# Performance work log

Hardware: AMD Instinct MI355X
Metric: run time of the kernel (lower is better)

## Reference

```python
import jax, jax.numpy as jnp
import numpy as np

N_NODES = 100000    # nodes in river network
N_PATHS = 1000000   # number of (src, dst) routing paths
MAX_DELAY = 16
DT = 1.0
CASCADE = 1.0
T = int(MAX_DELAY / DT)        # expanded time window (assert in original)
E = 8000000                    # total flattened path-node entries


def setup_inputs() -> dict:
    key = jax.random.key(0)
    k1, k2, k3 = jax.random.split(key, 3)
    params = jax.random.uniform(k1, (N_NODES,), dtype=jnp.float32)
    path_idxs = jnp.sort(jax.random.randint(k2, (E,), 0, N_PATHS, dtype=jnp.int32))
    path_nodes = jax.random.randint(k3, (E,), 0, N_NODES, dtype=jnp.int32)
    return {"params": params, "path_idxs": path_idxs, "path_nodes": path_nodes}


def reference(params, path_idxs, path_nodes):
    # irf_fn 'linear_storage': per-node linear-reservoir impulse response h(t)=exp(-t/k)/k
    k = params + 0.5                                  # storage const in [0.5, 1.5)
    t = jnp.arange(T, dtype=params.dtype) * DT        # [T]
    irfs = jnp.exp(-t[None, :] / k[:, None]) / k[:, None]   # [N, T]
    # frequency domain
    irfs_freq = jnp.fft.rfft(irfs, n=T, axis=-1)      # [N, F] complex
    # irf_agg 'log_triton': cascade-combine IRFs along each path = product of
    # transfer functions, done in log domain: gather logs, segment-sum per path.
    log_freq = jnp.log(irfs_freq)                     # [N, F] complex log
    gathered = log_freq[path_nodes]                   # [E, F] irregular gather
    agg_re = jax.ops.segment_sum(gathered.real, path_idxs, num_segments=N_PATHS)
    agg_im = jax.ops.segment_sum(gathered.imag, path_idxs, num_segments=N_PATHS)
    agg_log = (agg_re + 1j * agg_im) * CASCADE        # [P, F]
    irfs_freq_agg = jnp.exp(agg_log)
    # back to time domain
    irfs_agg = jnp.fft.irfft(irfs_freq_agg, n=T, axis=-1)   # [P, T]
    irfs_agg = jax.nn.relu(irfs_agg)
    irfs_agg = jnp.flip(irfs_agg, -1)                 # sampler.phi_k is identity for dt=1
    irfs_agg = irfs_agg / jnp.sum(irfs_agg, -1, keepdims=True)
    return irfs_agg                                   # COO values; coords scatter is a storage step
```

## Files before the change

kernel.cpp:

```cpp
#include <hip/hip_runtime.h>
#include <math.h>

#define N_NODES  100000
#define N_PATHS  1000000
#define E_TOT    8000000
#define NF       9
#define TAB_U32  25000
#define PN_CHUNK 10240
#define BLK      1024

#define RMIN 0.135330f
#define RMAX 0.513420f
#define QSCALE (255.0f / (RMAX - RMIN))
#define DEQ    ((RMAX - RMIN) / 255.0f)

__device__ __constant__ float COS16[16] = {
  1.0f,  0.92387953f,  0.70710678f,  0.38268343f,  0.0f, -0.38268343f, -0.70710678f, -0.92387953f,
 -1.0f, -0.92387953f, -0.70710678f, -0.38268343f,  0.0f,  0.38268343f,  0.70710678f,  0.92387953f };
__device__ __constant__ float SIN16[16] = {
  0.0f,  0.38268343f,  0.70710678f,  0.92387953f,  1.0f,  0.92387953f,  0.70710678f,  0.38268343f,
  0.0f, -0.38268343f, -0.70710678f, -0.92387953f, -1.0f, -0.92387953f, -0.70710678f, -0.38268343f };

__global__ void node_rq_kernel(const float* __restrict__ params,
                               unsigned char* __restrict__ rtab_q) {
    int n = blockIdx.x * blockDim.x + threadIdx.x;
    if (n >= N_NODES) return;
    float k = params[n] + 0.5f;
    float r = expf(-1.0f / k);
    float q = (r - RMIN) * QSCALE;
    q = fminf(fmaxf(q + 0.5f, 0.0f), 255.0f);
    rtab_q[n] = (unsigned char)q;
}

__device__ __forceinline__ void put_bounds(int a, int b, int e, int* __restrict__ start) {
    for (int p = a + 1; p <= b; ++p) start[p] = e;
}
__global__ void seg_starts_kernel(const int* __restrict__ pidx,
                                  int* __restrict__ start) {
    int q = blockIdx.x * blockDim.x + threadIdx.x;
    if (q >= E_TOT / 4) return;
    int e = q * 4;
    int4 v = ((const int4*)pidx)[q];
    int prev = (e == 0) ? -1 : pidx[e - 1];
    put_bounds(prev, v.x, e,     start);
    put_bounds(v.x,  v.y, e + 1, start);
    put_bounds(v.y,  v.z, e + 2, start);
    put_bounds(v.z,  v.w, e + 3, start);
    if (e + 4 == E_TOT) {
        for (int p = v.w + 1; p <= N_PATHS; ++p) start[p] = E_TOT;
    }
}

__global__ __launch_bounds__(BLK) void path_kernel(const int* __restrict__ start,
                                                   const int* __restrict__ pnode,
                                                   const unsigned int* __restrict__ rtab_q,
                                                   float* __restrict__ out) {
    __shared__ unsigned int tab[TAB_U32];
    __shared__ int pn[PN_CHUNK];
    const unsigned char* tabb = (const unsigned char*)tab;

    int tid = threadIdx.x;
    for (int i = tid; i < TAB_U32; i += BLK) tab[i] = rtab_q[i];

    int p0 = blockIdx.x * BLK;
    int p  = p0 + tid;
    int pend = (p0 + BLK < N_PATHS) ? p0 + BLK : N_PATHS;

    int blk_s = start[p0];
    int blk_e = start[pend];
    int s0 = 0, s1 = 0;
    if (p < N_PATHS) { s0 = start[p]; s1 = start[p + 1]; }

    float d0 = 1.0f, d8 = 1.0f;
    float dr[7], di[7];
#pragma unroll
    for (int f = 0; f < 7; f++) { dr[f] = 1.0f; di[f] = 0.0f; }

    for (int base = blk_s; base < blk_e; base += PN_CHUNK) {
        int len = (blk_e - base < PN_CHUNK) ? (blk_e - base) : PN_CHUNK;
        __syncthreads();
        for (int i = tid; i < len; i += BLK) pn[i] = pnode[base + i];
        __syncthreads();

        int lo = (s0 > base) ? s0 : base;
        int hi = (s1 < base + len) ? s1 : base + len;
        int e = lo;
        for (; e + 1 < hi; e += 2) {
            int na = pn[e - base];
            int nb = pn[e + 1 - base];
            float ra = fmaf((float)tabb[na], DEQ, RMIN);
            float rb = fmaf((float)tabb[nb], DEQ, RMIN);
#pragma unroll
            for (int f = 1; f <= 7; f++) {
                float cf = COS16[f], sf = SIN16[f];
                float t1r = fmaf(-ra, cf, 1.0f), t1i = ra * sf;
                float t2r = fmaf(-rb, cf, 1.0f), t2i = rb * sf;
                float tr = fmaf(t1r, t2r, -t1i * t2i);
                float ti = fmaf(t1r, t2i,  t1i * t2r);
                float a = dr[f - 1], b = di[f - 1];
                dr[f - 1] = fmaf(a, tr, -b * ti);
                di[f - 1] = fmaf(a, ti,  b * tr);
            }
            d0 *= (1.0f - ra) * (1.0f - rb);
            d8 *= (1.0f + ra) * (1.0f + rb);
        }
        if (e < hi) {
            int nn = pn[e - base];
            float r = fmaf((float)tabb[nn], DEQ, RMIN);
#pragma unroll
            for (int f = 1; f <= 7; f++) {
                float cf = COS16[f], sf = SIN16[f];
                float tr = fmaf(-r, cf, 1.0f), ti = r * sf;
                float a = dr[f - 1], b = di[f - 1];
                dr[f - 1] = fmaf(a, tr, -b * ti);
                di[f - 1] = fmaf(a, ti,  b * tr);
            }
            d0 = fmaf(-d0, r, d0);
            d8 = fmaf( d8, r, d8);
        }
    }

    if (p >= N_PATHS) return;

    float Xr[NF], Xi[NF];
    Xr[0] = 1.0f; Xi[0] = 0.0f;
#pragma unroll
    for (int f = 1; f < 8; f++) {
        float a = dr[f - 1], b = di[f - 1];
        float m = fmaf(a, a, b * b);
        float inv = d0 * __builtin_amdgcn_rcpf(m);
        Xr[f] =  a * inv;
        Xi[f] = -b * inv;
    }
    Xr[8] = d0 * __builtin_amdgcn_rcpf(d8); Xi[8] = 0.0f;

    float xt[16];
    float ssum = 0.0f;
#pragma unroll
    for (int t = 0; t < 16; t++) {
        float acc = Xr[0] + ((t & 1) ? -Xr[8] : Xr[8]);
#pragma unroll
        for (int f = 1; f < 8; f++) {
            int kk = (f * t) & 15;
            acc = fmaf(2.0f * Xr[f], COS16[kk], acc);
            acc = fmaf(-2.0f * Xi[f], SIN16[kk], acc);
        }
        acc *= (1.0f / 16.0f);
        acc = fmaxf(acc, 0.0f);
        xt[t] = acc;
        ssum += acc;
    }

    float invs = __builtin_amdgcn_rcpf(ssum);
    float4* op4 = (float4*)(out + (size_t)p * 16);
    op4[0] = make_float4(xt[15] * invs, xt[14] * invs, xt[13] * invs, xt[12] * invs);
    op4[1] = make_float4(xt[11] * invs, xt[10] * invs, xt[9]  * invs, xt[8]  * invs);
    op4[2] = make_float4(xt[7]  * invs, xt[6]  * invs, xt[5]  * invs, xt[4]  * invs);
    op4[3] = make_float4(xt[3]  * invs, xt[2]  * invs, xt[1]  * invs, xt[0]  * invs);
}

extern "C" void kernel_launch(void* const* d_in, const int* in_sizes, int n_in,
                              void* d_out, int out_size, void* d_ws, size_t ws_size,
                              hipStream_t stream) {
    const float* params = (const float*)d_in[0];
    const int* path_idxs = (const int*)d_in[1];
    const int* path_nodes = (const int*)d_in[2];
    float* out = (float*)d_out;

    size_t off_rq    = 0;
    size_t off_start = (off_rq + (size_t)N_NODES + 1023) & ~(size_t)1023;

    unsigned char* rtab_q = (unsigned char*)d_ws + off_rq;
    int* start = (int*)((char*)d_ws + off_start);

    {
        int threads = 256;
        int blocks = (N_NODES + threads - 1) / threads;
        node_rq_kernel<<<blocks, threads, 0, stream>>>(params, rtab_q);
    }
    {
        int threads = 256;
        int blocks = (E_TOT / 4 + threads - 1) / threads;
        seg_starts_kernel<<<blocks, threads, 0, stream>>>(path_idxs, start);
    }
    {
        int blocks = (N_PATHS + BLK - 1) / BLK;
        path_kernel<<<blocks, BLK, 0, stream>>>(start, path_nodes,
                                                (const unsigned int*)rtab_q, out);
    }
}
```

Baseline: 161.6 us.

## Pre-gather quantized node values per entry and batch four factors per step

The segment-start pass now also gathers each entry's quantized reservoir value into a byte array, so the path kernel streams 1 byte per entry instead of 4-byte node ids plus an LDS table lookup. The path kernel shrinks to 256-thread blocks without the 100KB table in shared memory, which allows more blocks per CU. It also multiplies four (1 - r z^-1) factors at once through their elementary symmetric polynomials instead of pairwise products, cutting per-entry FLOPs. The cost is an extra 8MB written and read back, plus a 100KB LDS table load in each block of the first pass.

```diff
diff --git a/kernel.cpp b/kernel.cpp
--- a/kernel.cpp
+++ b/kernel.cpp
@@ -6,8 +6,10 @@
 #define E_TOT    8000000
 #define NF       9
 #define TAB_U32  25000
-#define PN_CHUNK 10240
-#define BLK      1024
+#define EB       1024
+#define EPT      2
+#define PB       256
+#define RCH      4096
 
 #define RMIN 0.135330f
 #define RMAX 0.513420f
@@ -35,36 +37,51 @@
 __device__ __forceinline__ void put_bounds(int a, int b, int e, int* __restrict__ start) {
     for (int p = a + 1; p <= b; ++p) start[p] = e;
 }
-__global__ void seg_starts_kernel(const int* __restrict__ pidx,
-                                  int* __restrict__ start) {
-    int q = blockIdx.x * blockDim.x + threadIdx.x;
-    if (q >= E_TOT / 4) return;
-    int e = q * 4;
-    int4 v = ((const int4*)pidx)[q];
-    int prev = (e == 0) ? -1 : pidx[e - 1];
-    put_bounds(prev, v.x, e,     start);
-    put_bounds(v.x,  v.y, e + 1, start);
-    put_bounds(v.y,  v.z, e + 2, start);
-    put_bounds(v.z,  v.w, e + 3, start);
-    if (e + 4 == E_TOT) {
-        for (int p = v.w + 1; p <= N_PATHS; ++p) start[p] = E_TOT;
-    }
-}
-
-__global__ __launch_bounds__(BLK) void path_kernel(const int* __restrict__ start,
+
+__global__ __launch_bounds__(EB) void epass_kernel(const int* __restrict__ pidx,
                                                    const int* __restrict__ pnode,
                                                    const unsigned int* __restrict__ rtab_q,
-                                                   float* __restrict__ out) {
+                                                   int* __restrict__ start,
+                                                   unsigned char* __restrict__ r8_all) {
     __shared__ unsigned int tab[TAB_U32];
-    __shared__ int pn[PN_CHUNK];
     const unsigned char* tabb = (const unsigned char*)tab;
-
     int tid = threadIdx.x;
-    for (int i = tid; i < TAB_U32; i += BLK) tab[i] = rtab_q[i];
-
-    int p0 = blockIdx.x * BLK;
+    for (int i = tid; i < TAB_U32; i += EB) tab[i] = rtab_q[i];
+    __syncthreads();
+
+    int base_q = blockIdx.x * EB * EPT;
+#pragma unroll
+    for (int g = 0; g < EPT; g++) {
+        int q = base_q + g * EB + tid;
+        if (q >= E_TOT / 4) break;
+        int e = q * 4;
+        int4 v = ((const int4*)pidx)[q];
+        int4 w = ((const int4*)pnode)[q];
+        uchar4 r;
+        r.x = tabb[w.x];
+        r.y = tabb[w.y];
+        r.z = tabb[w.z];
+        r.w = tabb[w.w];
+        ((uchar4*)r8_all)[q] = r;
+        int prev = (e == 0) ? -1 : pidx[e - 1];
+        put_bounds(prev, v.x, e,     start);
+        put_bounds(v.x,  v.y, e + 1, start);
+        put_bounds(v.y,  v.z, e + 2, start);
+        put_bounds(v.z,  v.w, e + 3, start);
+        if (e + 4 == E_TOT) {
+            for (int p = v.w + 1; p <= N_PATHS; ++p) start[p] = E_TOT;
+        }
+    }
+}
+
+__global__ __launch_bounds__(PB) void path_kernel(const int* __restrict__ start,
+                                                  const unsigned char* __restrict__ r8_all,
+                                                  float* __restrict__ out) {
+    __shared__ unsigned char rch[RCH + 4];
+    int tid = threadIdx.x;
+    int p0 = blockIdx.x * PB;
     int p  = p0 + tid;
-    int pend = (p0 + BLK < N_PATHS) ? p0 + BLK : N_PATHS;
+    int pend = (p0 + PB < N_PATHS) ? p0 + PB : N_PATHS;
 
     int blk_s = start[p0];
     int blk_e = start[pend];
@@ -76,47 +93,46 @@
 #pragma unroll
     for (int f = 0; f < 7; f++) { dr[f] = 1.0f; di[f] = 0.0f; }
 
-    for (int base = blk_s; base < blk_e; base += PN_CHUNK) {
-        int len = (blk_e - base < PN_CHUNK) ? (blk_e - base) : PN_CHUNK;
+    const unsigned int* r8w = (const unsigned int*)r8_all;
+    for (int ab = blk_s & ~3; ab < blk_e; ab += RCH) {
+        int wlen = (blk_e - ab < RCH) ? (blk_e - ab) : RCH;
+        int nw = (wlen + 3) >> 2;
         __syncthreads();
-        for (int i = tid; i < len; i += BLK) pn[i] = pnode[base + i];
+        for (int j = tid; j < nw; j += PB)
+            ((unsigned int*)rch)[j] = r8w[(ab >> 2) + j];
         __syncthreads();
 
-        int lo = (s0 > base) ? s0 : base;
-        int hi = (s1 < base + len) ? s1 : base + len;
-        int e = lo;
-        for (; e + 1 < hi; e += 2) {
-            int na = pn[e - base];
-            int nb = pn[e + 1 - base];
-            float ra = fmaf((float)tabb[na], DEQ, RMIN);
-            float rb = fmaf((float)tabb[nb], DEQ, RMIN);
+        int lo = (s0 > ab) ? s0 : ab;
+        int hi = (s1 < ab + wlen) ? s1 : ab + wlen;
+        int n = hi - lo;
+        int bi = lo - ab;
+        for (int j = 0; j < n; j += 4) {
+            float ra = fmaf((float)rch[bi + j], DEQ, RMIN);
+            float rb = (j + 1 < n) ? fmaf((float)rch[bi + j + 1], DEQ, RMIN) : 0.0f;
+            float rc = (j + 2 < n) ? fmaf((float)rch[bi + j + 2], DEQ, RMIN) : 0.0f;
+            float rd = (j + 3 < n) ? fmaf((float)rch[bi + j + 3], DEQ, RMIN) : 0.0f;
+            float sab = ra + rb, qab = ra * rb;
+            float scd = rc + rd, qcd = rc * rd;
+            float e1 = sab + scd;
+            float e2 = fmaf(sab, scd, qab + qcd);
+            float e3 = fmaf(qab, scd, qcd * sab);
+            float e4 = qab * qcd;
 #pragma unroll
             for (int f = 1; f <= 7; f++) {
-                float cf = COS16[f], sf = SIN16[f];
-                float t1r = fmaf(-ra, cf, 1.0f), t1i = ra * sf;
-                float t2r = fmaf(-rb, cf, 1.0f), t2i = rb * sf;
-                float tr = fmaf(t1r, t2r, -t1i * t2i);
-                float ti = fmaf(t1r, t2i,  t1i * t2r);
+                float tr = fmaf(-e1, COS16[f], 1.0f);
+                tr = fmaf( e2, COS16[(2 * f) & 15], tr);
+                tr = fmaf(-e3, COS16[(3 * f) & 15], tr);
+                tr = fmaf( e4, COS16[(4 * f) & 15], tr);
+                float ti = e1 * SIN16[f];
+                ti = fmaf(-e2, SIN16[(2 * f) & 15], ti);
+                ti = fmaf( e3, SIN16[(3 * f) & 15], ti);
+                ti = fmaf(-e4, SIN16[(4 * f) & 15], ti);
                 float a = dr[f - 1], b = di[f - 1];
                 dr[f - 1] = fmaf(a, tr, -b * ti);
                 di[f - 1] = fmaf(a, ti,  b * tr);
             }
-            d0 *= (1.0f - ra) * (1.0f - rb);
-            d8 *= (1.0f + ra) * (1.0f + rb);
-        }
-        if (e < hi) {
-            int nn = pn[e - base];
-            float r = fmaf((float)tabb[nn], DEQ, RMIN);
-#pragma unroll
-            for (int f = 1; f <= 7; f++) {
-                float cf = COS16[f], sf = SIN16[f];
-                float tr = fmaf(-r, cf, 1.0f), ti = r * sf;
-                float a = dr[f - 1], b = di[f - 1];
-                dr[f - 1] = fmaf(a, tr, -b * ti);
-                di[f - 1] = fmaf(a, ti,  b * tr);
-            }
-            d0 = fmaf(-d0, r, d0);
-            d8 = fmaf( d8, r, d8);
+            d0 *= ((1.0f - e1) + (e2 - e3)) + e4;
+            d8 *= ((1.0f + e1) + (e2 + e3)) + e4;
         }
     }
 
@@ -169,9 +185,11 @@
 
     size_t off_rq    = 0;
     size_t off_start = (off_rq + (size_t)N_NODES + 1023) & ~(size_t)1023;
+    size_t off_r8    = (off_start + (size_t)(N_PATHS + 1) * 4 + 1023) & ~(size_t)1023;
 
     unsigned char* rtab_q = (unsigned char*)d_ws + off_rq;
     int* start = (int*)((char*)d_ws + off_start);
+    unsigned char* r8_all = (unsigned char*)d_ws + off_r8;
 
     {
         int threads = 256;
@@ -179,13 +197,14 @@
         node_rq_kernel<<<blocks, threads, 0, stream>>>(params, rtab_q);
     }
     {
-        int threads = 256;
-        int blocks = (E_TOT / 4 + threads - 1) / threads;
-        seg_starts_kernel<<<blocks, threads, 0, stream>>>(path_idxs, start);
+        int per_block = EB * EPT;
+        int blocks = (E_TOT / 4 + per_block - 1) / per_block;
+        epass_kernel<<<blocks, EB, 0, stream>>>(path_idxs, path_nodes,
+                                                (const unsigned int*)rtab_q,
+                                                start, r8_all);
     }
     {
-        int blocks = (N_PATHS + BLK - 1) / BLK;
-        path_kernel<<<blocks, BLK, 0, stream>>>(start, path_nodes,
-                                                (const unsigned int*)rtab_q, out);
-    }
-}
+        int blocks = (N_PATHS + PB - 1) / PB;
+        path_kernel<<<blocks, PB, 0, stream>>>(start, r8_all, out);
+    }
+}
```

Result: faster. 143.3 us (-11.3%).
